# Performance work log

Measured on AMD Instinct MI355X. Metric: run time of the kernel, lower is better.

## Reference

```python
import jax, jax.numpy as jnp
import numpy as np

# dims matching init_kwargs
NC_IN, NC_OUT = 32, 32
M_IN, M_OUT = 3, 3          # to_order(degree)=2*d+1 with degree=1
NUM_FREQ = 3                # to_order(min(degree_in, degree_out))
EDGE_DIM, MID_DIM = 32, 64  # mid_dim = int(edge_dim * radial_mult)
RAD_OUT = NUM_FREQ * NC_IN * NC_OUT  # 3072
LN_EPS = 1e-5


def _layernorm(x, g, b):
    mu = jnp.mean(x, axis=-1, keepdims=True)
    var = jnp.var(x, axis=-1, keepdims=True)
    return (x - mu) * jax.lax.rsqrt(var + LN_EPS) * g + b


def setup_inputs() -> dict:
    key = jax.random.key(0)
    ks = jax.random.split(key, 8)
    B, N, K = 1, 1024, 32
    edges = jax.random.normal(ks[0], (B, N, K, EDGE_DIM), dtype=jnp.float32)
    feats = jax.random.normal(ks[1], (B, N, K, NC_IN, M_IN), dtype=jnp.float32)
    basis = jax.random.normal(ks[2], (B * N * K, M_IN, NUM_FREQ * M_OUT), dtype=jnp.float32)
    # radial MLP params (Linear -> LN -> GELU) x2, then Linear (no bias since dropout=0)
    s1 = 1.0 / np.sqrt(EDGE_DIM)
    s2 = 1.0 / np.sqrt(MID_DIM)
    W1 = jax.random.uniform(ks[3], (EDGE_DIM, MID_DIM), jnp.float32, -s1, s1)
    b1 = jnp.zeros((MID_DIM,), jnp.float32)
    g1 = jnp.ones((MID_DIM,), jnp.float32)
    beta1 = jnp.zeros((MID_DIM,), jnp.float32)
    W2 = jax.random.uniform(ks[4], (MID_DIM, MID_DIM), jnp.float32, -s2, s2)
    b2 = jnp.zeros((MID_DIM,), jnp.float32)
    g2 = jnp.ones((MID_DIM,), jnp.float32)
    beta2 = jnp.zeros((MID_DIM,), jnp.float32)
    W3 = jax.random.uniform(ks[5], (MID_DIM, RAD_OUT), jnp.float32, -s2, s2)
    return dict(edges=edges, feats=feats, basis=basis, W1=W1, b1=b1, g1=g1,
                beta1=beta1, W2=W2, b2=b2, g2=g2, beta2=beta2, W3=W3)


def reference(edges, feats, basis, W1, b1, g1, beta1, W2, b2, g2, beta2, W3):
    B, N, K = feats.shape[:3]
    E = B * N * K
    # radial MLP: (E, edge_dim) -> (E, nc_out * nc_in * num_freq)
    x = edges.reshape(E, EDGE_DIM)
    h = jax.nn.gelu(_layernorm(x @ W1 + b1, g1, beta1), approximate=False)
    h = jax.nn.gelu(_layernorm(h @ W2 + b2, g2, beta2), approximate=False)
    rw = (h @ W3).reshape(E, NC_OUT, NC_IN * NUM_FREQ)  # rearrange '(o i f)' then flatten
    # feats @ basis: (E, nc_in, m_in) @ (E, m_in, num_freq*m_out)
    f = feats.reshape(E, NC_IN, M_IN)
    tmp = jnp.matmul(f, basis).reshape(E, NC_IN * NUM_FREQ, M_OUT)
    out = jnp.matmul(rw, tmp)  # (E, nc_out, m_out)
    return out.reshape(B, N, K, NC_OUT, M_OUT)
```

## Files before the change

kernel.cpp:

```cpp
#include <hip/hip_runtime.h>
#include <cstdint>
#include <cstddef>

typedef __bf16 bf8 __attribute__((ext_vector_type(8)));
typedef float f32x4 __attribute__((ext_vector_type(4)));
typedef unsigned short us8 __attribute__((ext_vector_type(8)));
typedef unsigned short us4 __attribute__((ext_vector_type(4)));

__device__ __forceinline__ uint16_t f2b(float f) {
    uint32_t u = __builtin_bit_cast(uint32_t, f);
    u += 0x7FFFu + ((u >> 16) & 1u);
    return (uint16_t)(u >> 16);
}
__device__ __forceinline__ float b2f(uint16_t h) {
    uint32_t u = ((uint32_t)h) << 16;
    return __builtin_bit_cast(float, u);
}

#define MFMA(a, b, c) __builtin_amdgcn_mfma_f32_16x16x32_bf16( \
    __builtin_bit_cast(bf8, (a)), __builtin_bit_cast(bf8, (b)), (c), 0, 0, 0)

__global__ void prep_weights(const float* __restrict__ W1,
                             const float* __restrict__ W2,
                             const float* __restrict__ W3,
                             uint16_t* __restrict__ wt) {
    int t = blockIdx.x * 256 + threadIdx.x;
    if (t < 2048) {
        int i = t >> 6, j = t & 63;
        wt[j * 32 + i] = f2b(W1[t]);
    } else if (t < 6144) {
        int t2 = t - 2048;
        int k = t2 >> 6, j = t2 & 63;
        wt[2048 + j * 64 + k] = f2b(W2[t2]);
    } else {
        int t3 = t - 6144;
        int k = t3 / 3072, j = t3 - k * 3072;
        wt[6144 + j * 64 + k] = f2b(W3[t3]);
    }
}

__global__ __launch_bounds__(256, 2) void pairconv_main(
    const float* __restrict__ edges, const float* __restrict__ feats,
    const float* __restrict__ basis,
    const float* __restrict__ b1, const float* __restrict__ g1, const float* __restrict__ be1,
    const float* __restrict__ b2, const float* __restrict__ g2, const float* __restrict__ be2,
    const uint16_t* __restrict__ wt, float* __restrict__ out) {

    __shared__ __align__(16) uint16_t sh_tmp[64 * 384];
    __shared__ __align__(16) uint16_t sh_h[64 * 64];
    __shared__ __align__(16) uint16_t sh_h1[4][16 * 64];

    const int tid = threadIdx.x;
    const int e0 = blockIdx.x * 64;
    const int lane = tid & 63, w = tid >> 6;
    const int n = lane & 15, q = lane >> 4;

    #pragma unroll
    for (int it = 0; it < 8; ++it) {
        int idx = tid + it * 256;
        int e = idx >> 5, i = idx & 31;
        const float* fp = feats + ((size_t)(e0 + e) * 32 + i) * 3;
        float f0 = fp[0], f1 = fp[1], f2v = fp[2];
        const float* bp = basis + (size_t)(e0 + e) * 27;
        #pragma unroll
        for (int f = 0; f < 3; ++f) {
            int c = i * 3 + f;
            int cq = c >> 2, cl = c & 3;
            us4 pk;
            #pragma unroll
            for (int m = 0; m < 3; ++m) {
                float v = f0 * bp[f * 3 + m] + f1 * bp[9 + f * 3 + m] + f2v * bp[18 + f * 3 + m];
                pk[m] = f2b(v);
            }
            pk[3] = 0;
            *(us4*)&sh_tmp[e * 384 + ((cq ^ (e & 7)) << 4) + cl * 4] = pk;
        }
    }
    __syncthreads();

    {
        const int eb = e0 + w * 16;
        us8 bx;
        {
            const float* xp = edges + (size_t)(eb + n) * 32 + q * 8;
            #pragma unroll
            for (int j = 0; j < 8; ++j) bx[j] = f2b(xp[j]);
        }
        f32x4 acc[4];
        #pragma unroll
        for (int mt = 0; mt < 4; ++mt) {
            us8 a = *(const us8*)(wt + (mt * 16 + n) * 32 + q * 8);
            f32x4 z = {0.f, 0.f, 0.f, 0.f};
            acc[mt] = MFMA(a, bx, z);
        }
        float v[4][4];
        float s1 = 0.f, s2 = 0.f;
        #pragma unroll
        for (int mt = 0; mt < 4; ++mt) {
            f32x4 bb = *(const f32x4*)&b1[mt * 16 + q * 4];
            #pragma unroll
            for (int r = 0; r < 4; ++r) {
                float x = acc[mt][r] + bb[r];
                v[mt][r] = x; s1 += x; s2 += x * x;
            }
        }
        s1 += __shfl_xor(s1, 16, 64); s1 += __shfl_xor(s1, 32, 64);
        s2 += __shfl_xor(s2, 16, 64); s2 += __shfl_xor(s2, 32, 64);
        float mean = s1 * (1.f / 64.f);
        float var  = s2 * (1.f / 64.f) - mean * mean;
        float rs = rsqrtf(var + 1e-5f);
        #pragma unroll
        for (int mt = 0; mt < 4; ++mt) {
            f32x4 gg = *(const f32x4*)&g1[mt * 16 + q * 4];
            f32x4 be = *(const f32x4*)&be1[mt * 16 + q * 4];
            us4 pk;
            #pragma unroll
            for (int r = 0; r < 4; ++r) {
                float y = (v[mt][r] - mean) * rs * gg[r] + be[r];
                float g = 0.5f * y * (1.f + erff(y * 0.70710678118654752f));
                pk[r] = f2b(g);
            }
            int kq = mt * 2 + (q >> 1);
            *(us4*)&sh_h1[w][n * 64 + ((kq ^ (n & 7)) << 3) + (q & 1) * 4] = pk;
        }
    }
    __syncthreads();
    {
        us8 bh0 = *(const us8*)&sh_h1[w][n * 64 + ((q ^ (n & 7)) << 3)];
        us8 bh1 = *(const us8*)&sh_h1[w][n * 64 + (((4 + q) ^ (n & 7)) << 3)];
        f32x4 acc[4];
        #pragma unroll
        for (int mt = 0; mt < 4; ++mt) {
            us8 a0 = *(const us8*)(wt + 2048 + (mt * 16 + n) * 64 + q * 8);
            us8 a1 = *(const us8*)(wt + 2048 + (mt * 16 + n) * 64 + 32 + q * 8);
            f32x4 z = {0.f, 0.f, 0.f, 0.f};
            acc[mt] = MFMA(a0, bh0, z);
            acc[mt] = MFMA(a1, bh1, acc[mt]);
        }
        float v[4][4]; float s1 = 0.f, s2 = 0.f;
        #pragma unroll
        for (int mt = 0; mt < 4; ++mt) {
            f32x4 bb = *(const f32x4*)&b2[mt * 16 + q * 4];
            #pragma unroll
            for (int r = 0; r < 4; ++r) {
                float x = acc[mt][r] + bb[r];
                v[mt][r] = x; s1 += x; s2 += x * x;
            }
        }
        s1 += __shfl_xor(s1, 16, 64); s1 += __shfl_xor(s1, 32, 64);
        s2 += __shfl_xor(s2, 16, 64); s2 += __shfl_xor(s2, 32, 64);
        float mean = s1 * (1.f / 64.f);
        float var  = s2 * (1.f / 64.f) - mean * mean;
        float rs = rsqrtf(var + 1e-5f);
        #pragma unroll
        for (int mt = 0; mt < 4; ++mt) {
            f32x4 gg = *(const f32x4*)&g2[mt * 16 + q * 4];
            f32x4 be = *(const f32x4*)&be2[mt * 16 + q * 4];
            us4 pk;
            #pragma unroll
            for (int r = 0; r < 4; ++r) {
                float y = (v[mt][r] - mean) * rs * gg[r] + be[r];
                float g = 0.5f * y * (1.f + erff(y * 0.70710678118654752f));
                pk[r] = f2b(g);
            }
            int e = w * 16 + n;
            int kq = mt * 2 + (q >> 1);
            *(us4*)&sh_h[e * 64 + ((kq ^ (e & 7)) << 3) + (q & 1) * 4] = pk;
        }
    }
    __syncthreads();

    {
        const uint16_t* w3t = wt + 6144;
        us8 bh[4][2];
        #pragma unroll
        for (int nt = 0; nt < 4; ++nt) {
            int e = nt * 16 + n;
            bh[nt][0] = *(const us8*)&sh_h[e * 64 + ((q ^ (e & 7)) << 3)];
            bh[nt][1] = *(const us8*)&sh_h[e * 64 + (((4 + q) ^ (e & 7)) << 3)];
        }
        const int ob = w * 8;
        #pragma unroll 1
        for (int oc = 0; oc < 2; ++oc) {
            float p[4][4][3];
            #pragma unroll
            for (int a = 0; a < 4; ++a)
                #pragma unroll
                for (int b = 0; b < 4; ++b)
                    #pragma unroll
                    for (int m = 0; m < 3; ++m) p[a][b][m] = 0.f;

            #pragma unroll 1
            for (int mt = 0; mt < 6; ++mt) {
                float ftmp[4][4][3];
                #pragma unroll
                for (int nt = 0; nt < 4; ++nt) {
                    int e = nt * 16 + n;
                    int cq = mt * 4 + q;
                    int base = e * 384 + ((cq ^ (e & 7)) << 4);
                    us8 t0 = *(const us8*)&sh_tmp[base];
                    us8 t1 = *(const us8*)&sh_tmp[base + 8];
                    #pragma unroll
                    for (int m = 0; m < 3; ++m) {
                        ftmp[nt][0][m] = b2f(t0[m]);
                        ftmp[nt][1][m] = b2f(t0[4 + m]);
                        ftmp[nt][2][m] = b2f(t1[m]);
                        ftmp[nt][3][m] = b2f(t1[4 + m]);
                    }
                }
                #pragma unroll
                for (int op = 0; op < 4; ++op) {
                    int o = ob + oc * 4 + op;
                    const uint16_t* ap = w3t + (size_t)(o * 96 + mt * 16 + n) * 64 + q * 8;
                    us8 a0 = *(const us8*)ap;
                    us8 a1 = *(const us8*)(ap + 32);
                    #pragma unroll
                    for (int nt = 0; nt < 4; ++nt) {
                        f32x4 z = {0.f, 0.f, 0.f, 0.f};
                        f32x4 acc = MFMA(a0, bh[nt][0], z);
                        acc = MFMA(a1, bh[nt][1], acc);
                        #pragma unroll
                        for (int r = 0; r < 4; ++r)
                            #pragma unroll
                            for (int m = 0; m < 3; ++m)
                                p[nt][op][m] += acc[r] * ftmp[nt][r][m];
                    }
                }
            }
            #pragma unroll
            for (int nt = 0; nt < 4; ++nt) {
                #pragma unroll
                for (int op = 0; op < 4; ++op) {
                    int o = ob + oc * 4 + op;
                    float v0 = p[nt][op][0], v1 = p[nt][op][1], v2 = p[nt][op][2];
                    v0 += __shfl_xor(v0, 16, 64); v0 += __shfl_xor(v0, 32, 64);
                    v1 += __shfl_xor(v1, 16, 64); v1 += __shfl_xor(v1, 32, 64);
                    v2 += __shfl_xor(v2, 16, 64); v2 += __shfl_xor(v2, 32, 64);
                    float val = (q == 0) ? v0 : ((q == 1) ? v1 : v2);
                    if (q < 3)
                        out[(size_t)(e0 + nt * 16 + n) * 96 + o * 3 + q] = val;
                }
            }
        }
    }
}

extern "C" void kernel_launch(void* const* d_in, const int* in_sizes, int n_in,
                              void* d_out, int out_size, void* d_ws, size_t ws_size,
                              hipStream_t stream) {
    const float* edges = (const float*)d_in[0];
    const float* feats = (const float*)d_in[1];
    const float* basis = (const float*)d_in[2];
    const float* W1  = (const float*)d_in[3];
    const float* b1  = (const float*)d_in[4];
    const float* g1  = (const float*)d_in[5];
    const float* be1 = (const float*)d_in[6];
    const float* W2  = (const float*)d_in[7];
    const float* b2  = (const float*)d_in[8];
    const float* g2  = (const float*)d_in[9];
    const float* be2 = (const float*)d_in[10];
    const float* W3  = (const float*)d_in[11];
    uint16_t* wt = (uint16_t*)d_ws;
    float* out = (float*)d_out;

    const int E = in_sizes[0] / 32;
    hipLaunchKernelGGL(prep_weights, dim3(792), dim3(256), 0, stream, W1, W2, W3, wt);
    hipLaunchKernelGGL(pairconv_main, dim3(E / 64), dim3(256), 0, stream,
                       edges, feats, basis, b1, g1, be1, b2, g2, be2, wt, out);
}
```

Measured before the change: 132.1 us.

## Tile W3 transpose, vectorize loads, fast GELU, drop redundant barriers

The weight-prep kernel now transposes W3 through a padded shared-memory tile, so both global reads and writes are coalesced, and it launches far fewer blocks. In the main kernel, edges are loaded early as float4, feats and basis are read with vector loads, and the sh_tmp swizzle moves to 8-element granularity. Two __syncthreads that only guarded wave-local or later-synchronised data are removed. The erf-based GELU becomes a tanh-form approximation built on exp and a hardware reciprocal, and rsqrtf becomes the raw hardware rsq. The approximate GELU differs slightly from the exact erf GELU the reference specifies.

```diff
diff --git a/kernel.cpp b/kernel.cpp
--- a/kernel.cpp
+++ b/kernel.cpp
@@ -4,6 +4,8 @@
 
 typedef __bf16 bf8 __attribute__((ext_vector_type(8)));
 typedef float f32x4 __attribute__((ext_vector_type(4)));
+typedef float f32x4u __attribute__((ext_vector_type(4), aligned(4)));
+typedef float f32x3u __attribute__((ext_vector_type(3), aligned(4)));
 typedef unsigned short us8 __attribute__((ext_vector_type(8)));
 typedef unsigned short us4 __attribute__((ext_vector_type(4)));
 
@@ -16,6 +18,12 @@
     uint32_t u = ((uint32_t)h) << 16;
     return __builtin_bit_cast(float, u);
 }
+__device__ __forceinline__ float gelu_fast(float y) {
+    float y3 = y * y * y;
+    float z2 = 1.5957691216f * (y + 0.044715f * y3);
+    float u = __expf(-z2);
+    return y * __builtin_amdgcn_rcpf(1.0f + u);
+}
 
 #define MFMA(a, b, c) __builtin_amdgcn_mfma_f32_16x16x32_bf16( \
     __builtin_bit_cast(bf8, (a)), __builtin_bit_cast(bf8, (b)), (c), 0, 0, 0)
@@ -24,18 +32,31 @@
                              const float* __restrict__ W2,
                              const float* __restrict__ W3,
                              uint16_t* __restrict__ wt) {
-    int t = blockIdx.x * 256 + threadIdx.x;
-    if (t < 2048) {
-        int i = t >> 6, j = t & 63;
-        wt[j * 32 + i] = f2b(W1[t]);
-    } else if (t < 6144) {
-        int t2 = t - 2048;
-        int k = t2 >> 6, j = t2 & 63;
-        wt[2048 + j * 64 + k] = f2b(W2[t2]);
+    __shared__ float tile[32][33];
+    int bx = blockIdx.x;
+    if (bx < 192) {
+        int kb = (bx & 1) * 32;
+        int jb = (bx >> 1) * 32;
+        int tx = threadIdx.x & 31, ty = threadIdx.x >> 5;
+        #pragma unroll
+        for (int l = 0; l < 4; ++l)
+            tile[ty + 8 * l][tx] = W3[(size_t)(kb + ty + 8 * l) * 3072 + jb + tx];
+        __syncthreads();
+        #pragma unroll
+        for (int l = 0; l < 4; ++l) {
+            int j = jb + ty + 8 * l;
+            wt[6144 + (size_t)j * 64 + kb + tx] = f2b(tile[tx][ty + 8 * l]);
+        }
     } else {
-        int t3 = t - 6144;
-        int k = t3 / 3072, j = t3 - k * 3072;
-        wt[6144 + j * 64 + k] = f2b(W3[t3]);
+        int t = (bx - 192) * 256 + threadIdx.x;
+        if (t < 2048) {
+            int i = t >> 6, j = t & 63;
+            wt[j * 32 + i] = f2b(W1[t]);
+        } else {
+            int t2 = t - 2048;
+            int k = t2 >> 6, j = t2 & 63;
+            wt[2048 + j * 64 + k] = f2b(W2[t2]);
+        }
     }
 }
 
@@ -55,37 +76,43 @@
     const int lane = tid & 63, w = tid >> 6;
     const int n = lane & 15, q = lane >> 4;
 
+    const int eb = e0 + w * 16;
+    f32x4 ex0 = *(const f32x4*)(edges + (size_t)(eb + n) * 32 + q * 8);
+    f32x4 ex1 = *(const f32x4*)(edges + (size_t)(eb + n) * 32 + q * 8 + 4);
+
     #pragma unroll
     for (int it = 0; it < 8; ++it) {
         int idx = tid + it * 256;
         int e = idx >> 5, i = idx & 31;
-        const float* fp = feats + ((size_t)(e0 + e) * 32 + i) * 3;
-        float f0 = fp[0], f1 = fp[1], f2v = fp[2];
-        const float* bp = basis + (size_t)(e0 + e) * 27;
+        f32x3u fv = *(const f32x3u*)(feats + ((size_t)(e0 + e) * 32 + i) * 3);
+        const float* bpp = basis + (size_t)(e0 + e) * 27;
+        float bp[27];
+        #pragma unroll
+        for (int v = 0; v < 6; ++v) {
+            f32x4u t = *(const f32x4u*)(bpp + v * 4);
+            bp[v * 4] = t[0]; bp[v * 4 + 1] = t[1]; bp[v * 4 + 2] = t[2]; bp[v * 4 + 3] = t[3];
+        }
+        bp[24] = bpp[24]; bp[25] = bpp[25]; bp[26] = bpp[26];
+        int sw = e & 7;
         #pragma unroll
         for (int f = 0; f < 3; ++f) {
             int c = i * 3 + f;
-            int cq = c >> 2, cl = c & 3;
+            int u = c >> 1;
             us4 pk;
             #pragma unroll
             for (int m = 0; m < 3; ++m) {
-                float v = f0 * bp[f * 3 + m] + f1 * bp[9 + f * 3 + m] + f2v * bp[18 + f * 3 + m];
+                float v = fv[0] * bp[f * 3 + m] + fv[1] * bp[9 + f * 3 + m] + fv[2] * bp[18 + f * 3 + m];
                 pk[m] = f2b(v);
             }
             pk[3] = 0;
-            *(us4*)&sh_tmp[e * 384 + ((cq ^ (e & 7)) << 4) + cl * 4] = pk;
-        }
-    }
-    __syncthreads();
+            *(us4*)&sh_tmp[e * 384 + ((u ^ sw) << 3) + (c & 1) * 4] = pk;
+        }
+    }
 
     {
-        const int eb = e0 + w * 16;
         us8 bx;
-        {
-            const float* xp = edges + (size_t)(eb + n) * 32 + q * 8;
-            #pragma unroll
-            for (int j = 0; j < 8; ++j) bx[j] = f2b(xp[j]);
-        }
+        #pragma unroll
+        for (int j = 0; j < 4; ++j) { bx[j] = f2b(ex0[j]); bx[4 + j] = f2b(ex1[j]); }
         f32x4 acc[4];
         #pragma unroll
         for (int mt = 0; mt < 4; ++mt) {
@@ -108,7 +135,7 @@
         s2 += __shfl_xor(s2, 16, 64); s2 += __shfl_xor(s2, 32, 64);
         float mean = s1 * (1.f / 64.f);
         float var  = s2 * (1.f / 64.f) - mean * mean;
-        float rs = rsqrtf(var + 1e-5f);
+        float rs = __builtin_amdgcn_rsqf(var + 1e-5f);
         #pragma unroll
         for (int mt = 0; mt < 4; ++mt) {
             f32x4 gg = *(const f32x4*)&g1[mt * 16 + q * 4];
@@ -117,14 +144,12 @@
             #pragma unroll
             for (int r = 0; r < 4; ++r) {
                 float y = (v[mt][r] - mean) * rs * gg[r] + be[r];
-                float g = 0.5f * y * (1.f + erff(y * 0.70710678118654752f));
-                pk[r] = f2b(g);
+                pk[r] = f2b(gelu_fast(y));
             }
             int kq = mt * 2 + (q >> 1);
             *(us4*)&sh_h1[w][n * 64 + ((kq ^ (n & 7)) << 3) + (q & 1) * 4] = pk;
         }
     }
-    __syncthreads();
     {
         us8 bh0 = *(const us8*)&sh_h1[w][n * 64 + ((q ^ (n & 7)) << 3)];
         us8 bh1 = *(const us8*)&sh_h1[w][n * 64 + (((4 + q) ^ (n & 7)) << 3)];
@@ -151,7 +176,7 @@
         s2 += __shfl_xor(s2, 16, 64); s2 += __shfl_xor(s2, 32, 64);
         float mean = s1 * (1.f / 64.f);
         float var  = s2 * (1.f / 64.f) - mean * mean;
-        float rs = rsqrtf(var + 1e-5f);
+        float rs = __builtin_amdgcn_rsqf(var + 1e-5f);
         #pragma unroll
         for (int mt = 0; mt < 4; ++mt) {
             f32x4 gg = *(const f32x4*)&g2[mt * 16 + q * 4];
@@ -160,8 +185,7 @@
             #pragma unroll
             for (int r = 0; r < 4; ++r) {
                 float y = (v[mt][r] - mean) * rs * gg[r] + be[r];
-                float g = 0.5f * y * (1.f + erff(y * 0.70710678118654752f));
-                pk[r] = f2b(g);
+                pk[r] = f2b(gelu_fast(y));
             }
             int e = w * 16 + n;
             int kq = mt * 2 + (q >> 1);
@@ -196,10 +220,10 @@
                 #pragma unroll
                 for (int nt = 0; nt < 4; ++nt) {
                     int e = nt * 16 + n;
-                    int cq = mt * 4 + q;
-                    int base = e * 384 + ((cq ^ (e & 7)) << 4);
-                    us8 t0 = *(const us8*)&sh_tmp[base];
-                    us8 t1 = *(const us8*)&sh_tmp[base + 8];
+                    int u0 = mt * 8 + q * 2;
+                    int sw = e & 7;
+                    us8 t0 = *(const us8*)&sh_tmp[e * 384 + ((u0 ^ sw) << 3)];
+                    us8 t1 = *(const us8*)&sh_tmp[e * 384 + (((u0 + 1) ^ sw) << 3)];
                     #pragma unroll
                     for (int m = 0; m < 3; ++m) {
                         ftmp[nt][0][m] = b2f(t0[m]);
@@ -264,7 +288,7 @@
     float* out = (float*)d_out;
 
     const int E = in_sizes[0] / 32;
-    hipLaunchKernelGGL(prep_weights, dim3(792), dim3(256), 0, stream, W1, W2, W3, wt);
+    hipLaunchKernelGGL(prep_weights, dim3(216), dim3(256), 0, stream, W1, W2, W3, wt);
     hipLaunchKernelGGL(pairconv_main, dim3(E / 64), dim3(256), 0, stream,
                        edges, feats, basis, b1, g1, be1, b2, g2, be2, wt, out);
 }
```

Measured after the change: 130.4 us. Within noise of the previous version (-1.3%).
